# Performance work log

Measured on AMD Instinct MI355X. Metric: run time of the kernel, lower is better.

## Reference

```python
import jax, jax.numpy as jnp
import numpy as np

NUM_BINS = 36
EPS = 1e-12
BASE_DROP, MIN_DROP, MAX_DROP = 0.3, 0.1, 0.6
SENSITIVITY, NORMAL_APE = 4.0, 0.78


def _hann(n):
    # torch.hann_window default (periodic=True): 0.5*(1 - cos(2*pi*k/N))
    return 0.5 - 0.5 * jnp.cos(2.0 * jnp.pi * jnp.arange(n, dtype=jnp.float32) / n)


def compute_ape(images):
    B, C, H, W = images.shape
    mean = jnp.array([0.485, 0.456, 0.406], dtype=images.dtype).reshape(1, 3, 1, 1)
    std = jnp.array([0.229, 0.224, 0.225], dtype=images.dtype).reshape(1, 3, 1, 1)
    wts = jnp.array([0.2989, 0.587, 0.114], dtype=images.dtype).reshape(1, 3, 1, 1)
    gray = ((images * std + mean) * wts).sum(axis=1)  # (B,H,W)
    gray = gray - gray.mean(axis=(1, 2), keepdims=True)
    gray = gray * (_hann(H)[:, None] * _hann(W)[None, :])
    P = jnp.abs(jnp.fft.fft2(gray)) ** 2
    P = jnp.fft.fftshift(P, axes=(1, 2))
    cy, cx = (H - 1) / 2.0, (W - 1) / 2.0
    yy = jnp.arange(H, dtype=jnp.float32)[:, None] - cy
    xx = jnp.arange(W, dtype=jnp.float32)[None, :] - cx
    r = jnp.sqrt(xx ** 2 + yy ** 2)
    theta = (jnp.arctan2(yy, xx) + 2 * jnp.pi) % (2 * jnp.pi)
    r_max = r.max()
    radial_mask = (r >= 0.05 * r_max) & (r <= 0.95 * r_max)
    bin_width = 2 * jnp.pi / NUM_BINS
    idx = jnp.clip((theta / bin_width).astype(jnp.int32), 0, NUM_BINS - 1)  # (H,W)
    # batched masked angular histogram: one segment_sum over B*NUM_BINS segments
    Pm = (P * radial_mask).reshape(B, -1)
    seg = (idx.reshape(-1)[None, :] + NUM_BINS * jnp.arange(B)[:, None]).reshape(-1)
    energy = jax.ops.segment_sum(Pm.reshape(-1), seg, num_segments=B * NUM_BINS)
    energy = energy.reshape(B, NUM_BINS)
    total = energy.sum(axis=1, keepdims=True)
    p = energy / (total + EPS)
    H_theta = -(p * jnp.log(p + EPS)).sum(axis=1)
    ape = jnp.clip(H_theta / np.log(NUM_BINS), 0.0, 1.0)
    return jnp.where(total[:, 0] <= EPS, 0.0, ape)


def ape_to_dropout_prob(ape):
    adj = jnp.tanh((NORMAL_APE - ape) * SENSITIVITY)
    drop = jnp.where(adj >= 0,
                     BASE_DROP + adj * (MAX_DROP - BASE_DROP),
                     BASE_DROP + adj * (BASE_DROP - MIN_DROP))
    return jnp.clip(drop, MIN_DROP, MAX_DROP)


def adaptive_dropout(x, probs, key):
    # per-sample dropout: mask ~ Bernoulli(1-p), scale by 1/(1-p+1e-8)
    p = probs[:, None, None]
    keep = jax.random.bernoulli(key, 1.0 - p, x.shape).astype(x.dtype)
    out = x * keep / (1.0 - p + 1e-8)
    return jnp.where(p > 0, out, x)


def setup_inputs() -> dict:
    key = jax.random.key(0)
    k1, k2, k3, k4 = jax.random.split(key, 4)
    B, N, D, Hf = 64, 256, 768, 768
    images = jax.random.uniform(k1, (B, 3, 448, 448), dtype=jnp.float32)
    x = jax.random.normal(k2, (B, N, D), dtype=jnp.float32)
    w1 = jax.random.normal(k3, (Hf, D), dtype=jnp.float32) * (1.0 / np.sqrt(D))
    w2 = jax.random.normal(k4, (D, Hf), dtype=jnp.float32) * (1.0 / np.sqrt(Hf))
    return {"images": images, "x": x, "w1": w1, "w2": w2}


def reference(images, x, w1, w2):
    ape = compute_ape(images)
    probs = jax.lax.stop_gradient(ape_to_dropout_prob(ape))  # torch casts to python float -> detached
    k0, k1, k2 = jax.random.split(jax.random.key(1), 3)
    h = adaptive_dropout(x, probs, k0)            # input dropout
    h = jnp.einsum('bnd,hd->bnh', h, w1)          # fc1 (bias=False)
    h = jax.nn.gelu(h, approximate=False)         # nn.GELU (exact erf)
    h = adaptive_dropout(h, probs, k1)
    y = jnp.einsum('bnh,dh->bnd', h, w2)          # fc2 (bias=False)
    y = adaptive_dropout(y, probs, k2)
    return y
```

## Files before the change

### kernel.cpp

```cpp
#include <hip/hip_runtime.h>
#include <stdint.h>
#include <math.h>

typedef __attribute__((ext_vector_type(8))) short short8;
typedef __attribute__((ext_vector_type(4))) float floatx4;

#define IMGN 448
#define HW   200704
#define NBATCH 64
#define NBINS 36

#define MFMA(a, b, c) __builtin_amdgcn_mfma_f32_16x16x32_bf16((a), (b), (c), 0, 0, 0)

#define WS_WIN   0u
#define WS_BINS  4096u
#define WS_TS    24576u
#define WS_BIDX  32768u
#define WS_TW    1048576u
#define TWSZ     401408u
#define WS_W     4194304u
#define WSZ      1179648u
#define WS_REG1  16777216u
#define GSZ      25690112u
#define CBSZ     13762560u
#define XSZ      25165824u
#define WS_REG2  75497472u
#define CRSZ     29360128u

__host__ __device__ __forceinline__ uint32_t rotl32(uint32_t v, int r) {
  return (v << r) | (v >> (32 - r));
}
__host__ __device__ __forceinline__ void tf2x32(uint32_t k0, uint32_t k1,
                                                uint32_t x0, uint32_t x1,
                                                uint32_t &o0, uint32_t &o1) {
  uint32_t k2 = k0 ^ k1 ^ 0x1BD11BDAu;
  uint32_t v0 = x0 + k0, v1 = x1 + k1;
#define TFR(r) { v0 += v1; v1 = rotl32(v1, r); v1 ^= v0; }
  TFR(13) TFR(15) TFR(26) TFR(6)   v0 += k1; v1 += k2 + 1u;
  TFR(17) TFR(29) TFR(16) TFR(24)  v0 += k2; v1 += k0 + 2u;
  TFR(13) TFR(15) TFR(26) TFR(6)   v0 += k0; v1 += k1 + 3u;
  TFR(17) TFR(29) TFR(16) TFR(24)  v0 += k1; v1 += k2 + 4u;
  TFR(13) TFR(15) TFR(26) TFR(6)   v0 += k2; v1 += k0 + 5u;
#undef TFR
  o0 = v0; o1 = v1;
}
__device__ __forceinline__ float tf_uniform(uint32_t k0, uint32_t k1, uint32_t idx) {
  uint32_t a, b;
  tf2x32(k0, k1, 0u, idx, a, b);
  uint32_t bits = a ^ b;
  return __uint_as_float((bits >> 9) | 0x3F800000u) - 1.0f;
}

__device__ __forceinline__ unsigned short bf16rne(float v) {
  unsigned u = __float_as_uint(v);
  return (unsigned short)((u + 0x7fffu + ((u >> 16) & 1u)) >> 16);
}
__device__ __forceinline__ void split2(float v, unsigned short &h, unsigned short &l) {
  h = bf16rne(v);
  float fh = __uint_as_float(((unsigned)h) << 16);
  l = bf16rne(v - fh);
}

__device__ __forceinline__ void gload16(const void *g, void *l) {
  __builtin_amdgcn_global_load_lds(
      (const __attribute__((address_space(1))) unsigned int *)g,
      (__attribute__((address_space(3))) unsigned int *)l, 16, 0, 0);
}

__global__ __launch_bounds__(256) void k_prep(float *__restrict__ win,
                                              double *__restrict__ bins,
                                              uint8_t *__restrict__ bidx) {
  int t = blockIdx.x * 256 + threadIdx.x;
  int a = t / IMGN, b = t % IMGN;
  double yy = (double)((a + 224) % IMGN) - 223.5;
  double xx = (double)((b + 224) % IMGN) - 223.5;
  double r2 = xx * xx + yy * yy;
  uint8_t idx = 255;
  if (r2 >= 249.76125 && r2 <= 90163.81125) {
    double th = atan2(yy, xx);
    if (th < 0.0) th += 6.283185307179586476925286766559;
    int i = (int)(th / 0.17453292519943295769236907684886);
    if (i > 35) i = 35;
    if (i < 0) i = 0;
    idx = (uint8_t)i;
  }
  bidx[t] = idx;
  if (t < IMGN) {
    double ang = 6.283185307179586476925286766559 * (double)t / 448.0;
    win[t] = (float)(0.5 - 0.5 * cos(ang));
  }
  if (t < NBATCH * NBINS) bins[t] = 0.0;
}

__global__ __launch_bounds__(256) void k_tw(short8 *__restrict__ tch, short8 *__restrict__ tcl,
                                            short8 *__restrict__ tsh, short8 *__restrict__ tsl) {
  int wid = blockIdx.x * 256 + threadIdx.x;
  int lane = wid & 63;
  int tmp = wid >> 6;
  int kb = tmp % 14, mb = tmp / 14;
  int m = mb * 16 + (lane & 15);
  int k0 = kb * 32 + (lane >> 4) * 8;
  short8 ch, cl, sh, sl;
#pragma unroll
  for (int e = 0; e < 8; ++e) {
    int mm = (m * (k0 + e)) % IMGN;
    double ang = -6.283185307179586476925286766559 * (double)mm / 448.0;
    float c = (float)cos(ang), s = (float)sin(ang);
    unsigned short h, l;
    split2(c, h, l); ch[e] = (short)h; cl[e] = (short)l;
    split2(s, h, l); sh[e] = (short)h; sl[e] = (short)l;
  }
  tch[wid] = ch; tcl[wid] = cl; tsh[wid] = sh; tsl[wid] = sl;
}

__global__ __launch_bounds__(256) void k_wconv(const float *__restrict__ w1, const float *__restrict__ w2,
                                               short8 *__restrict__ w1h, short8 *__restrict__ w1l,
                                               short8 *__restrict__ w2h, short8 *__restrict__ w2l) {
  int wid = blockIdx.x * 256 + threadIdx.x;
  const float *src = blockIdx.y ? w2 : w1;
  short8 *dh = blockIdx.y ? w2h : w1h;
  short8 *dl = blockIdx.y ? w2l : w1l;
  int lane = wid & 63;
  int tmp = wid >> 6;
  int kb = tmp % 24, nb = tmp / 24;
  int n = nb * 16 + (lane & 15);
  int k0 = kb * 32 + (lane >> 4) * 8;
  const float *p = src + (size_t)n * 768 + k0;
  short8 vh, vl;
#pragma unroll
  for (int e = 0; e < 8; ++e) {
    unsigned short h, l;
    split2(p[e], h, l);
    vh[e] = (short)h; vl[e] = (short)l;
  }
  dh[wid] = vh; dl[wid] = vl;
}

__global__ __launch_bounds__(256) void k_gprep(const float *__restrict__ img, const float *__restrict__ win,
                                               short8 *__restrict__ gh, short8 *__restrict__ gl) {
  int wid = blockIdx.x * 256 + threadIdx.x;
  int lane = wid & 63;
  int tmp = wid >> 6;
  int kb = tmp % 14, nb = tmp / 14;
  int n = nb * 16 + (lane & 15);
  int b = n / 448, y = n % 448;
  int x0 = kb * 32 + (lane >> 4) * 8;
  const float *p = img + (size_t)b * 3 * HW + y * IMGN + x0;
  float wy = win[y];
  short8 vh, vl;
#pragma unroll
  for (int e = 0; e < 8; ++e) {
    float r = p[e], g = p[HW + e], bl = p[2 * HW + e];
    float t0 = (r * 0.229f + 0.485f) * 0.2989f;
    float t1 = (g * 0.224f + 0.456f) * 0.587f;
    float t2 = (bl * 0.225f + 0.406f) * 0.114f;
    float v = ((t0 + t1) + t2) * wy * win[x0 + e];
    unsigned short h, l;
    split2(v, h, l);
    vh[e] = (short)h; vl[e] = (short)l;
  }
  gh[wid] = vh; gl[wid] = vl;
}

__global__ __launch_bounds__(256) void k_rows(const short8 *__restrict__ tch, const short8 *__restrict__ tcl,
                                              const short8 *__restrict__ tsh, const short8 *__restrict__ tsl,
                                              const short8 *__restrict__ gh, const short8 *__restrict__ gl,
                                              float *__restrict__ cr, float *__restrict__ ci) {
  __shared__ short8 S[1536];
  int orig = blockIdx.x;
  int swz = (orig & 7) * 224 + (orig >> 3);
  int mtg = swz & 3, ntg = swz >> 2;
  int tid = threadIdx.x;
  int lane = tid & 63, w = tid >> 6;
  int g = lane >> 4, c = lane & 15;
  floatx4 s_c[4] = {}, s_s[4] = {};
  for (int kb = 0; kb < 14; ++kb) {
#pragma unroll
    for (int i = 0; i < 6; ++i) {
      int ch = w * 6 + i;
      const short8 *m0;
      int row;
      if (ch < 16) {
        int sel = ch >> 2;
        m0 = sel == 0 ? tch : sel == 1 ? tcl : sel == 2 ? tsh : tsl;
        row = mtg * 4 + (ch & 3);
      } else {
        int cc = ch - 16;
        m0 = (cc >> 2) ? gl : gh;
        row = ntg * 4 + (cc & 3);
      }
      gload16(m0 + ((size_t)row * 14 + kb) * 64 + lane, (char *)S + ch * 1024);
    }
    __syncthreads();
    int ao = w * 64 + lane;
    short8 ach = S[0 * 256 + ao], acl = S[1 * 256 + ao];
    short8 ash = S[2 * 256 + ao], asl = S[3 * 256 + ao];
#pragma unroll
    for (int nt = 0; nt < 4; ++nt) {
      short8 bh = S[1024 + nt * 64 + lane];
      short8 bl = S[1280 + nt * 64 + lane];
      s_c[nt] = MFMA(ach, bh, s_c[nt]);
      s_c[nt] = MFMA(ach, bl, s_c[nt]);
      s_c[nt] = MFMA(acl, bh, s_c[nt]);
      s_s[nt] = MFMA(ash, bh, s_s[nt]);
      s_s[nt] = MFMA(ash, bl, s_s[nt]);
      s_s[nt] = MFMA(asl, bh, s_s[nt]);
    }
    __syncthreads();
  }
#pragma unroll
  for (int nt = 0; nt < 4; ++nt) {
    int n = (ntg * 4 + nt) * 16 + c;
#pragma unroll
    for (int r = 0; r < 4; ++r) {
      int v = (mtg * 4 + w) * 16 + 4 * g + r;
      cr[(size_t)v * 28672 + n] = s_c[nt][r];
      ci[(size_t)v * 28672 + n] = s_s[nt][r];
    }
  }
}

__global__ __launch_bounds__(256) void k_repack(const float *__restrict__ cr, const float *__restrict__ ci,
                                                short8 *__restrict__ crh, short8 *__restrict__ crl,
                                                short8 *__restrict__ cih, short8 *__restrict__ cil) {
  int wid = blockIdx.x * 256 + threadIdx.x;
  int lane = wid & 63;
  int tmp = wid >> 6;
  int kb = tmp % 14, nb = tmp / 14;
  int n = nb * 16 + (lane & 15);
  int b = n / 240, v = n % 240;
  int y0 = kb * 32 + (lane >> 4) * 8;
  const float *pr = cr + (size_t)v * 28672 + b * 448 + y0;
  const float *pi = ci + (size_t)v * 28672 + b * 448 + y0;
  short8 rh, rl, ih, il;
#pragma unroll
  for (int e = 0; e < 8; ++e) {
    unsigned short h, l;
    split2(pr[e], h, l); rh[e] = (short)h; rl[e] = (short)l;
    split2(pi[e], h, l); ih[e] = (short)h; il[e] = (short)l;
  }
  crh[wid] = rh; crl[wid] = rl; cih[wid] = ih; cil[wid] = il;
}

__global__ __launch_bounds__(256) void k_cols(const short8 *__restrict__ tch, const short8 *__restrict__ tcl,
                                              const short8 *__restrict__ tsh, const short8 *__restrict__ tsl,
                                              const short8 *__restrict__ crh, const short8 *__restrict__ crl,
                                              const short8 *__restrict__ cih, const short8 *__restrict__ cil,
                                              const uint8_t *__restrict__ bidx, double *__restrict__ bins) {
  __shared__ short8 S[2048];
  __shared__ double lb[72];
  int orig = blockIdx.x;
  int swz = (orig & 7) * 210 + (orig >> 3);
  int mtg = swz % 7, ntg = swz / 7;
  int tid = threadIdx.x;
  if (tid < 72) lb[tid] = 0.0;
  int lane = tid & 63, w = tid >> 6;
  int g = lane >> 4, c = lane & 15;
  floatx4 s_cc[4] = {}, s_sc[4] = {}, s_ss[4] = {}, s_cs[4] = {};
  for (int kb = 0; kb < 14; ++kb) {
#pragma unroll
    for (int i = 0; i < 8; ++i) {
      int ch = w * 8 + i;
      int sel = ch >> 2;
      const short8 *m0 = sel == 0 ? tch : sel == 1 ? tcl : sel == 2 ? tsh : sel == 3 ? tsl
                       : sel == 4 ? crh : sel == 5 ? crl : sel == 6 ? cih : cil;
      int row = (sel < 4) ? (mtg * 4 + (ch & 3)) : (ntg * 4 + (ch & 3));
      gload16(m0 + ((size_t)row * 14 + kb) * 64 + lane, (char *)S + ch * 1024);
    }
    __syncthreads();
    int ao = w * 64 + lane;
    short8 ach = S[0 * 256 + ao], acl = S[1 * 256 + ao];
    short8 ash = S[2 * 256 + ao], asl = S[3 * 256 + ao];
#pragma unroll
    for (int nt = 0; nt < 4; ++nt) {
      short8 brh = S[1024 + nt * 64 + lane];
      short8 brl = S[1280 + nt * 64 + lane];
      short8 bih = S[1536 + nt * 64 + lane];
      short8 bil = S[1792 + nt * 64 + lane];
      s_cc[nt] = MFMA(ach, brh, s_cc[nt]);
      s_cc[nt] = MFMA(ach, brl, s_cc[nt]);
      s_cc[nt] = MFMA(acl, brh, s_cc[nt]);
      s_sc[nt] = MFMA(ash, brh, s_sc[nt]);
      s_sc[nt] = MFMA(ash, brl, s_sc[nt]);
      s_sc[nt] = MFMA(asl, brh, s_sc[nt]);
      s_ss[nt] = MFMA(ash, bih, s_ss[nt]);
      s_ss[nt] = MFMA(ash, bil, s_ss[nt]);
      s_ss[nt] = MFMA(asl, bih, s_ss[nt]);
      s_cs[nt] = MFMA(ach, bih, s_cs[nt]);
      s_cs[nt] = MFMA(ach, bil, s_cs[nt]);
      s_cs[nt] = MFMA(acl, bih, s_cs[nt]);
    }
    __syncthreads();
  }
  int base_b = (ntg * 64) / 240;
#pragma unroll
  for (int nt = 0; nt < 4; ++nt) {
    int n = (ntg * 4 + nt) * 16 + c;
    int v = n % 240;
    int bloc = n / 240 - base_b;
    if (v < 225) {
#pragma unroll
      for (int r = 0; r < 4; ++r) {
        int u = (mtg * 4 + w) * 16 + 4 * g + r;
        float frv = s_cc[nt][r] - s_ss[nt][r];
        float fiv = s_sc[nt][r] + s_cs[nt][r];
        double P = (double)frv * frv + (double)fiv * fiv;
        int i1 = bidx[u * IMGN + v];
        if (i1 < 36) atomicAdd(&lb[bloc * 36 + i1], P);
        if (v >= 1 && v <= 223) {
          int i2 = bidx[((IMGN - u) % IMGN) * IMGN + (IMGN - v)];
          if (i2 < 36) atomicAdd(&lb[bloc * 36 + i2], P);
        }
      }
    }
  }
  __syncthreads();
  if (tid < 72) {
    int bb = base_b + tid / 36;
    if (bb < NBATCH && lb[tid] != 0.0) atomicAdd(&bins[bb * NBINS + (tid % 36)], lb[tid]);
  }
}

__global__ void k_probs(const double *__restrict__ bins, float *__restrict__ ts) {
  int b = threadIdx.x;
  if (b >= NBATCH) return;
  double T = 0.0;
  for (int i = 0; i < NBINS; ++i) T += bins[b * NBINS + i];
  double H = 0.0;
  for (int i = 0; i < NBINS; ++i) {
    double p = bins[b * NBINS + i] / (T + 1e-12);
    H -= p * log(p + 1e-12);
  }
  double ape = H / 3.5835189384561099;
  if (ape > 1.0) ape = 1.0;
  if (ape < 0.0) ape = 0.0;
  if (T <= 1e-12) ape = 0.0;
  double adj = tanh((0.78 - ape) * 4.0);
  double drop = (adj >= 0.0) ? (0.3 + adj * 0.3) : (0.3 + adj * 0.2);
  if (drop < 0.1) drop = 0.1;
  if (drop > 0.6) drop = 0.6;
  float p32 = (float)drop;
  ts[b] = 1.0f - p32;
  ts[NBATCH + b] = 1.0f / (1.0f - p32 + 1e-8f);
}

__global__ __launch_bounds__(256) void k_dropfrag(const float *__restrict__ x, const float *__restrict__ ts,
                                                  short8 *__restrict__ xh, short8 *__restrict__ xl,
                                                  uint32_t k0, uint32_t k1) {
  int wid = blockIdx.x * 256 + threadIdx.x;
  int lane = wid & 63;
  int tmp = wid >> 6;
  int kb = tmp % 24, mb = tmp / 24;
  int m = mb * 16 + (lane & 15);
  int d0 = kb * 32 + (lane >> 4) * 8;
  int bi = m >> 8;
  float t = ts[bi], s = ts[NBATCH + bi];
  const float *p = x + (size_t)m * 768 + d0;
  short8 vh, vl;
#pragma unroll
  for (int e = 0; e < 8; ++e) {
    uint32_t idx = (uint32_t)m * 768u + (uint32_t)(d0 + e);
    float u = tf_uniform(k0, k1, idx);
    float v = (u < t) ? p[e] * s : 0.0f;
    unsigned short h, l;
    split2(v, h, l);
    vh[e] = (short)h; vl[e] = (short)l;
  }
  xh[wid] = vh; xl[wid] = vl;
}

template <int MODE>
__global__ __launch_bounds__(256) void k_mlp(const short8 *__restrict__ ah, const short8 *__restrict__ al,
                                             const short8 *__restrict__ bh, const short8 *__restrict__ bl,
                                             const float *__restrict__ ts, float *__restrict__ out,
                                             short8 *__restrict__ oh, short8 *__restrict__ ol,
                                             uint32_t k0, uint32_t k1) {
  __shared__ short8 S[1024];
  int orig = blockIdx.x;
  int swz = (orig & 7) * 384 + (orig >> 3);
  int ntg = swz % 12, mtg = swz / 12;
  int tid = threadIdx.x;
  int lane = tid & 63, w = tid >> 6;
  int g = lane >> 4, c = lane & 15;
  floatx4 acc[4] = {};
  for (int kb = 0; kb < 24; ++kb) {
#pragma unroll
    for (int i = 0; i < 4; ++i) {
      int ch = w * 4 + i;
      int sel = ch >> 2;
      const short8 *m0 = sel == 0 ? ah : sel == 1 ? al : sel == 2 ? bh : bl;
      int row = (sel < 2) ? (mtg * 4 + (ch & 3)) : (ntg * 4 + (ch & 3));
      gload16(m0 + ((size_t)row * 24 + kb) * 64 + lane, (char *)S + ch * 1024);
    }
    __syncthreads();
    int ao = w * 64 + lane;
    short8 a_h = S[0 * 256 + ao], a_l = S[1 * 256 + ao];
#pragma unroll
    for (int nt = 0; nt < 4; ++nt) {
      short8 b_h = S[512 + nt * 64 + lane];
      short8 b_l = S[768 + nt * 64 + lane];
      acc[nt] = MFMA(a_h, b_h, acc[nt]);
      acc[nt] = MFMA(a_h, b_l, acc[nt]);
      acc[nt] = MFMA(a_l, b_h, acc[nt]);
    }
    __syncthreads();
  }
#pragma unroll
  for (int nt = 0; nt < 4; ++nt) {
    int n = (ntg * 4 + nt) * 16 + c;
#pragma unroll
    for (int r = 0; r < 4; ++r) {
      int m = (mtg * 4 + w) * 16 + 4 * g + r;
      float val = acc[nt][r];
      if (MODE == 1)
        val = 0.5f * val * (1.0f + erff(val * 0.70710678118654752440f));
      int bi = m >> 8;
      float t = ts[bi], s = ts[NBATCH + bi];
      uint32_t idx = (uint32_t)m * 768u + (uint32_t)n;
      float u = tf_uniform(k0, k1, idx);
      val = (u < t) ? val * s : 0.0f;
      if (MODE == 1) {
        unsigned short hh, hl;
        split2(val, hh, hl);
        int kb2 = n >> 5;
        int lane2 = (m & 15) + 16 * ((n & 31) >> 3);
        int e2 = n & 7;
        size_t word = ((size_t)(m >> 4) * 24 + kb2) * 64 + lane2;
        ((unsigned short *)oh)[word * 8 + e2] = hh;
        ((unsigned short *)ol)[word * 8 + e2] = hl;
      } else {
        out[(size_t)m * 768 + n] = val;
      }
    }
  }
}

extern "C" void kernel_launch(void *const *d_in, const int *in_sizes, int n_in,
                              void *d_out, int out_size, void *d_ws, size_t ws_size,
                              hipStream_t stream) {
  (void)in_sizes; (void)n_in; (void)out_size; (void)ws_size;
  const float *images = (const float *)d_in[0];
  const float *x  = (const float *)d_in[1];
  const float *w1 = (const float *)d_in[2];
  const float *w2 = (const float *)d_in[3];

  char *ws = (char *)d_ws;
  float   *win  = (float *)  (ws + WS_WIN);
  double  *bins = (double *) (ws + WS_BINS);
  float   *ts   = (float *)  (ws + WS_TS);
  uint8_t *bidx = (uint8_t *)(ws + WS_BIDX);
  short8  *tch  = (short8 *) (ws + WS_TW + 0 * TWSZ);
  short8  *tcl  = (short8 *) (ws + WS_TW + 1 * TWSZ);
  short8  *tsh  = (short8 *) (ws + WS_TW + 2 * TWSZ);
  short8  *tsl  = (short8 *) (ws + WS_TW + 3 * TWSZ);
  short8  *w1h  = (short8 *) (ws + WS_W + 0 * WSZ);
  short8  *w1l  = (short8 *) (ws + WS_W + 1 * WSZ);
  short8  *w2h  = (short8 *) (ws + WS_W + 2 * WSZ);
  short8  *w2l  = (short8 *) (ws + WS_W + 3 * WSZ);
  short8  *gh   = (short8 *) (ws + WS_REG1 + 0 * GSZ);
  short8  *gl   = (short8 *) (ws + WS_REG1 + 1 * GSZ);
  short8  *crh  = (short8 *) (ws + WS_REG1 + 0 * CBSZ);
  short8  *crl  = (short8 *) (ws + WS_REG1 + 1 * CBSZ);
  short8  *cih  = (short8 *) (ws + WS_REG1 + 2 * CBSZ);
  short8  *cil  = (short8 *) (ws + WS_REG1 + 3 * CBSZ);
  short8  *xh   = (short8 *) (ws + WS_REG1 + 0 * XSZ);
  short8  *xl   = (short8 *) (ws + WS_REG1 + 1 * XSZ);
  float   *cr   = (float *)  (ws + WS_REG2 + 0 * CRSZ);
  float   *ci   = (float *)  (ws + WS_REG2 + 1 * CRSZ);
  short8  *hh_  = (short8 *) (ws + WS_REG2 + 0 * XSZ);
  short8  *hl_  = (short8 *) (ws + WS_REG2 + 1 * XSZ);
  float   *yout = (float *)d_out;

  uint32_t keys[6];
  tf2x32(0u, 1u, 0u, 0u, keys[0], keys[1]);
  tf2x32(0u, 1u, 0u, 1u, keys[2], keys[3]);
  tf2x32(0u, 1u, 0u, 2u, keys[4], keys[5]);

  k_prep<<<784, 256, 0, stream>>>(win, bins, bidx);
  k_tw<<<98, 256, 0, stream>>>(tch, tcl, tsh, tsl);
  k_wconv<<<dim3(288, 2), 256, 0, stream>>>(w1, w2, w1h, w1l, w2h, w2l);
  k_gprep<<<6272, 256, 0, stream>>>(images, win, gh, gl);
  k_rows<<<1792, 256, 0, stream>>>(tch, tcl, tsh, tsl, gh, gl, cr, ci);
  k_repack<<<3360, 256, 0, stream>>>(cr, ci, crh, crl, cih, cil);
  k_cols<<<1680, 256, 0, stream>>>(tch, tcl, tsh, tsl, crh, crl, cih, cil, bidx, bins);
  k_probs<<<1, 64, 0, stream>>>(bins, ts);
  k_dropfrag<<<6144, 256, 0, stream>>>(x, ts, xh, xl, keys[0], keys[1]);
  k_mlp<1><<<3072, 256, 0, stream>>>(xh, xl, w1h, w1l, ts, yout, hh_, hl_, keys[2], keys[3]);
  k_mlp<2><<<3072, 256, 0, stream>>>(hh_, hl_, w2h, w2l, ts, yout, hh_, hl_, keys[4], keys[5]);
}
```

Measured before the change: 470.0 us.

## Double-buffer LDS tiles in row, column and MLP GEMM kernels

The row-DFT, column-DFT and MLP GEMM kernels now double-buffer their shared-memory tiles. Each kernel loads the first K-block before the loop, then issues the global-to-LDS loads for the next K-block before running the MFMAs on the current buffer. This lets global memory latency overlap with matrix compute instead of stalling on a barrier each iteration. In exchange, shared memory per block doubles, which may lower occupancy. The barrier's wait for outstanding loads may also limit how much overlap is actually achieved.

```diff
diff --git a/kernel.cpp b/kernel.cpp
--- a/kernel.cpp
+++ b/kernel.cpp
@@ -166,7 +166,7 @@
                                               const short8 *__restrict__ tsh, const short8 *__restrict__ tsl,
                                               const short8 *__restrict__ gh, const short8 *__restrict__ gl,
                                               float *__restrict__ cr, float *__restrict__ ci) {
-  __shared__ short8 S[1536];
+  __shared__ short8 S[2][1536];
   int orig = blockIdx.x;
   int swz = (orig & 7) * 224 + (orig >> 3);
   int mtg = swz & 3, ntg = swz >> 2;
@@ -174,31 +174,41 @@
   int lane = tid & 63, w = tid >> 6;
   int g = lane >> 4, c = lane & 15;
   floatx4 s_c[4] = {}, s_s[4] = {};
+
+#define ROWS_STAGE(buf, kb)                                                    \
+  {                                                                            \
+    _Pragma("unroll")                                                          \
+    for (int i = 0; i < 6; ++i) {                                              \
+      int ch = w * 6 + i;                                                      \
+      const short8 *m0;                                                        \
+      int row;                                                                 \
+      if (ch < 16) {                                                           \
+        int sel = ch >> 2;                                                     \
+        m0 = sel == 0 ? tch : sel == 1 ? tcl : sel == 2 ? tsh : tsl;           \
+        row = mtg * 4 + (ch & 3);                                              \
+      } else {                                                                 \
+        int cc = ch - 16;                                                      \
+        m0 = (cc >> 2) ? gl : gh;                                              \
+        row = ntg * 4 + (cc & 3);                                              \
+      }                                                                        \
+      gload16(m0 + ((size_t)row * 14 + (kb)) * 64 + lane,                      \
+              (char *)&S[buf][0] + ch * 1024);                                 \
+    }                                                                          \
+  }
+
+  ROWS_STAGE(0, 0);
+  __syncthreads();
   for (int kb = 0; kb < 14; ++kb) {
-#pragma unroll
-    for (int i = 0; i < 6; ++i) {
-      int ch = w * 6 + i;
-      const short8 *m0;
-      int row;
-      if (ch < 16) {
-        int sel = ch >> 2;
-        m0 = sel == 0 ? tch : sel == 1 ? tcl : sel == 2 ? tsh : tsl;
-        row = mtg * 4 + (ch & 3);
-      } else {
-        int cc = ch - 16;
-        m0 = (cc >> 2) ? gl : gh;
-        row = ntg * 4 + (cc & 3);
-      }
-      gload16(m0 + ((size_t)row * 14 + kb) * 64 + lane, (char *)S + ch * 1024);
-    }
-    __syncthreads();
+    int cur = kb & 1;
+    if (kb < 13) ROWS_STAGE(cur ^ 1, kb + 1);
+    const short8 *Sc = &S[cur][0];
     int ao = w * 64 + lane;
-    short8 ach = S[0 * 256 + ao], acl = S[1 * 256 + ao];
-    short8 ash = S[2 * 256 + ao], asl = S[3 * 256 + ao];
+    short8 ach = Sc[0 * 256 + ao], acl = Sc[1 * 256 + ao];
+    short8 ash = Sc[2 * 256 + ao], asl = Sc[3 * 256 + ao];
 #pragma unroll
     for (int nt = 0; nt < 4; ++nt) {
-      short8 bh = S[1024 + nt * 64 + lane];
-      short8 bl = S[1280 + nt * 64 + lane];
+      short8 bh = Sc[1024 + nt * 64 + lane];
+      short8 bl = Sc[1280 + nt * 64 + lane];
       s_c[nt] = MFMA(ach, bh, s_c[nt]);
       s_c[nt] = MFMA(ach, bl, s_c[nt]);
       s_c[nt] = MFMA(acl, bh, s_c[nt]);
@@ -247,7 +257,7 @@
                                               const short8 *__restrict__ crh, const short8 *__restrict__ crl,
                                               const short8 *__restrict__ cih, const short8 *__restrict__ cil,
                                               const uint8_t *__restrict__ bidx, double *__restrict__ bins) {
-  __shared__ short8 S[2048];
+  __shared__ short8 S[2][2048];
   __shared__ double lb[72];
   int orig = blockIdx.x;
   int swz = (orig & 7) * 210 + (orig >> 3);
@@ -257,26 +267,37 @@
   int lane = tid & 63, w = tid >> 6;
   int g = lane >> 4, c = lane & 15;
   floatx4 s_cc[4] = {}, s_sc[4] = {}, s_ss[4] = {}, s_cs[4] = {};
+
+#define COLS_STAGE(buf, kb)                                                    \
+  {                                                                            \
+    _Pragma("unroll")                                                          \
+    for (int i = 0; i < 8; ++i) {                                              \
+      int ch = w * 8 + i;                                                      \
+      int sel = ch >> 2;                                                       \
+      const short8 *m0 = sel == 0 ? tch : sel == 1 ? tcl : sel == 2 ? tsh      \
+                       : sel == 3 ? tsl : sel == 4 ? crh : sel == 5 ? crl      \
+                       : sel == 6 ? cih : cil;                                 \
+      int row = (sel < 4) ? (mtg * 4 + (ch & 3)) : (ntg * 4 + (ch & 3));       \
+      gload16(m0 + ((size_t)row * 14 + (kb)) * 64 + lane,                      \
+              (char *)&S[buf][0] + ch * 1024);                                 \
+    }                                                                          \
+  }
+
+  COLS_STAGE(0, 0);
+  __syncthreads();
   for (int kb = 0; kb < 14; ++kb) {
-#pragma unroll
-    for (int i = 0; i < 8; ++i) {
-      int ch = w * 8 + i;
-      int sel = ch >> 2;
-      const short8 *m0 = sel == 0 ? tch : sel == 1 ? tcl : sel == 2 ? tsh : sel == 3 ? tsl
-                       : sel == 4 ? crh : sel == 5 ? crl : sel == 6 ? cih : cil;
-      int row = (sel < 4) ? (mtg * 4 + (ch & 3)) : (ntg * 4 + (ch & 3));
-      gload16(m0 + ((size_t)row * 14 + kb) * 64 + lane, (char *)S + ch * 1024);
-    }
-    __syncthreads();
+    int cur = kb & 1;
+    if (kb < 13) COLS_STAGE(cur ^ 1, kb + 1);
+    const short8 *Sc = &S[cur][0];
     int ao = w * 64 + lane;
-    short8 ach = S[0 * 256 + ao], acl = S[1 * 256 + ao];
-    short8 ash = S[2 * 256 + ao], asl = S[3 * 256 + ao];
+    short8 ach = Sc[0 * 256 + ao], acl = Sc[1 * 256 + ao];
+    short8 ash = Sc[2 * 256 + ao], asl = Sc[3 * 256 + ao];
 #pragma unroll
     for (int nt = 0; nt < 4; ++nt) {
-      short8 brh = S[1024 + nt * 64 + lane];
-      short8 brl = S[1280 + nt * 64 + lane];
-      short8 bih = S[1536 + nt * 64 + lane];
-      short8 bil = S[1792 + nt * 64 + lane];
+      short8 brh = Sc[1024 + nt * 64 + lane];
+      short8 brl = Sc[1280 + nt * 64 + lane];
+      short8 bih = Sc[1536 + nt * 64 + lane];
+      short8 bil = Sc[1792 + nt * 64 + lane];
       s_cc[nt] = MFMA(ach, brh, s_cc[nt]);
       s_cc[nt] = MFMA(ach, brl, s_cc[nt]);
       s_cc[nt] = MFMA(acl, brh, s_cc[nt]);
@@ -375,7 +396,7 @@
                                              const float *__restrict__ ts, float *__restrict__ out,
                                              short8 *__restrict__ oh, short8 *__restrict__ ol,
                                              uint32_t k0, uint32_t k1) {
-  __shared__ short8 S[1024];
+  __shared__ short8 S[2][1024];
   int orig = blockIdx.x;
   int swz = (orig & 7) * 384 + (orig >> 3);
   int ntg = swz % 12, mtg = swz / 12;
@@ -383,22 +404,32 @@
   int lane = tid & 63, w = tid >> 6;
   int g = lane >> 4, c = lane & 15;
   floatx4 acc[4] = {};
+
+#define MLP_STAGE(buf, kb)                                                     \
+  {                                                                            \
+    _Pragma("unroll")                                                          \
+    for (int i = 0; i < 4; ++i) {                                              \
+      int ch = w * 4 + i;                                                      \
+      int sel = ch >> 2;                                                       \
+      const short8 *m0 = sel == 0 ? ah : sel == 1 ? al : sel == 2 ? bh : bl;   \
+      int row = (sel < 2) ? (mtg * 4 + (ch & 3)) : (ntg * 4 + (ch & 3));       \
+      gload16(m0 + ((size_t)row * 24 + (kb)) * 64 + lane,                      \
+              (char *)&S[buf][0] + ch * 1024);                                 \
+    }                                                                          \
+  }
+
+  MLP_STAGE(0, 0);
+  __syncthreads();
   for (int kb = 0; kb < 24; ++kb) {
-#pragma unroll
-    for (int i = 0; i < 4; ++i) {
-      int ch = w * 4 + i;
-      int sel = ch >> 2;
-      const short8 *m0 = sel == 0 ? ah : sel == 1 ? al : sel == 2 ? bh : bl;
-      int row = (sel < 2) ? (mtg * 4 + (ch & 3)) : (ntg * 4 + (ch & 3));
-      gload16(m0 + ((size_t)row * 24 + kb) * 64 + lane, (char *)S + ch * 1024);
-    }
-    __syncthreads();
+    int cur = kb & 1;
+    if (kb < 23) MLP_STAGE(cur ^ 1, kb + 1);
+    const short8 *Sc = &S[cur][0];
     int ao = w * 64 + lane;
-    short8 a_h = S[0 * 256 + ao], a_l = S[1 * 256 + ao];
+    short8 a_h = Sc[0 * 256 + ao], a_l = Sc[1 * 256 + ao];
 #pragma unroll
     for (int nt = 0; nt < 4; ++nt) {
-      short8 b_h = S[512 + nt * 64 + lane];
-      short8 b_l = S[768 + nt * 64 + lane];
+      short8 b_h = Sc[512 + nt * 64 + lane];
+      short8 b_l = Sc[768 + nt * 64 + lane];
       acc[nt] = MFMA(a_h, b_h, acc[nt]);
       acc[nt] = MFMA(a_h, b_l, acc[nt]);
       acc[nt] = MFMA(a_l, b_h, acc[nt]);
```

Result: slower. 506.4 us (+7.7%).

## Replace atomic shared-memory binning in column FFT with separate deterministic binning kernel

Applied to the files above, without the earlier changes.

The column-DFT kernel no longer accumulates power into per-block shared-memory double bins with atomics. It now writes the half-spectrum power as a float array to workspace. A new kernel then loads per-pixel bin indices, gathers power for each batch image using Hermitian symmetry, and reduces four bins per block with a shared-memory tree. This removes contended double-precision LDS atomics from the MFMA kernel, at the cost of an extra launch and a write and read of a roughly 26 MB power buffer. The new kernel also scans the full bin-index map nine times per image.

```diff
diff --git a/kernel.cpp b/kernel.cpp
--- a/kernel.cpp
+++ b/kernel.cpp
@@ -246,14 +246,12 @@
                                               const short8 *__restrict__ tsh, const short8 *__restrict__ tsl,
                                               const short8 *__restrict__ crh, const short8 *__restrict__ crl,
                                               const short8 *__restrict__ cih, const short8 *__restrict__ cil,
-                                              const uint8_t *__restrict__ bidx, double *__restrict__ bins) {
+                                              float *__restrict__ P) {
   __shared__ short8 S[2048];
-  __shared__ double lb[72];
   int orig = blockIdx.x;
   int swz = (orig & 7) * 210 + (orig >> 3);
   int mtg = swz % 7, ntg = swz / 7;
   int tid = threadIdx.x;
-  if (tid < 72) lb[tid] = 0.0;
   int lane = tid & 63, w = tid >> 6;
   int g = lane >> 4, c = lane & 15;
   floatx4 s_cc[4] = {}, s_sc[4] = {}, s_ss[4] = {}, s_cs[4] = {};
@@ -292,32 +290,68 @@
     }
     __syncthreads();
   }
-  int base_b = (ntg * 64) / 240;
 #pragma unroll
   for (int nt = 0; nt < 4; ++nt) {
     int n = (ntg * 4 + nt) * 16 + c;
     int v = n % 240;
-    int bloc = n / 240 - base_b;
+    int b = n / 240;
     if (v < 225) {
 #pragma unroll
       for (int r = 0; r < 4; ++r) {
         int u = (mtg * 4 + w) * 16 + 4 * g + r;
         float frv = s_cc[nt][r] - s_ss[nt][r];
         float fiv = s_sc[nt][r] + s_cs[nt][r];
-        double P = (double)frv * frv + (double)fiv * fiv;
-        int i1 = bidx[u * IMGN + v];
-        if (i1 < 36) atomicAdd(&lb[bloc * 36 + i1], P);
-        if (v >= 1 && v <= 223) {
-          int i2 = bidx[((IMGN - u) % IMGN) * IMGN + (IMGN - v)];
-          if (i2 < 36) atomicAdd(&lb[bloc * 36 + i2], P);
+        P[((size_t)b * 448 + u) * 225 + v] = frv * frv + fiv * fiv;
+      }
+    }
+  }
+}
+
+__global__ __launch_bounds__(256) void k_bins(const float *__restrict__ P,
+                                              const uint8_t *__restrict__ bidx,
+                                              double *__restrict__ bins) {
+  int grp = blockIdx.x;
+  int b = blockIdx.y;
+  int tid = threadIdx.x;
+  const float *Pb = P + (size_t)b * 100800;
+  double a0 = 0.0, a1 = 0.0, a2 = 0.0, a3 = 0.0;
+  for (int cb = tid; cb < 12544; cb += 256) {
+    int u = cb / 28;
+    int v0 = (cb - u * 28) * 16;
+    const uint32_t *q = (const uint32_t *)(bidx + (size_t)u * IMGN + v0);
+    int rb1 = u * 225;
+    int rb2 = ((IMGN - u) % IMGN) * 225;
+#pragma unroll
+    for (int wq = 0; wq < 4; ++wq) {
+      uint32_t wv = q[wq];
+#pragma unroll
+      for (int e = 0; e < 4; ++e) {
+        int bv = (wv >> (8 * e)) & 0xFF;
+        if ((bv >> 2) == grp) {
+          int v = v0 + wq * 4 + e;
+          int p = (v < 225) ? (rb1 + v) : (rb2 + (IMGN - v));
+          double d = (double)Pb[p];
+          int s = bv & 3;
+          a0 += (s == 0) ? d : 0.0;
+          a1 += (s == 1) ? d : 0.0;
+          a2 += (s == 2) ? d : 0.0;
+          a3 += (s == 3) ? d : 0.0;
         }
       }
     }
   }
-  __syncthreads();
-  if (tid < 72) {
-    int bb = base_b + tid / 36;
-    if (bb < NBATCH && lb[tid] != 0.0) atomicAdd(&bins[bb * NBINS + (tid % 36)], lb[tid]);
+  __shared__ double sd[256];
+#pragma unroll
+  for (int a = 0; a < 4; ++a) {
+    double v = (a == 0) ? a0 : (a == 1) ? a1 : (a == 2) ? a2 : a3;
+    sd[tid] = v;
+    __syncthreads();
+    for (int s = 128; s > 0; s >>= 1) {
+      if (tid < s) sd[tid] += sd[tid + s];
+      __syncthreads();
+    }
+    if (tid == 0) bins[b * NBINS + grp * 4 + a] = sd[0];
+    __syncthreads();
   }
 }
 
@@ -467,6 +501,7 @@
   short8  *xl   = (short8 *) (ws + WS_REG1 + 1 * XSZ);
   float   *cr   = (float *)  (ws + WS_REG2 + 0 * CRSZ);
   float   *ci   = (float *)  (ws + WS_REG2 + 1 * CRSZ);
+  float   *Pw   = (float *)  (ws + WS_REG2);
   short8  *hh_  = (short8 *) (ws + WS_REG2 + 0 * XSZ);
   short8  *hl_  = (short8 *) (ws + WS_REG2 + 1 * XSZ);
   float   *yout = (float *)d_out;
@@ -482,7 +517,8 @@
   k_gprep<<<6272, 256, 0, stream>>>(images, win, gh, gl);
   k_rows<<<1792, 256, 0, stream>>>(tch, tcl, tsh, tsl, gh, gl, cr, ci);
   k_repack<<<3360, 256, 0, stream>>>(cr, ci, crh, crl, cih, cil);
-  k_cols<<<1680, 256, 0, stream>>>(tch, tcl, tsh, tsl, crh, crl, cih, cil, bidx, bins);
+  k_cols<<<1680, 256, 0, stream>>>(tch, tcl, tsh, tsl, crh, crl, cih, cil, Pw);
+  k_bins<<<dim3(9, 64), 256, 0, stream>>>(Pw, bidx, bins);
   k_probs<<<1, 64, 0, stream>>>(bins, ts);
   k_dropfrag<<<6144, 256, 0, stream>>>(x, ts, xh, xl, keys[0], keys[1]);
   k_mlp<1><<<3072, 256, 0, stream>>>(xh, xl, w1h, w1l, ts, yout, hh_, hl_, keys[2], keys[3]);
```

Result: slower. 595.8 us (+26.8%).
